# Optimization experiments

Hardware: AMD Instinct MI355X
Metric: run time of the kernel (lower is better)

## Reference

```python
import jax, jax.numpy as jnp
import numpy as np

C = 512
CQK = C // 8
B, H, W = 4, 128, 128

def setup_inputs() -> dict:
    key = jax.random.key(0)
    ks = jax.random.split(key, 8)
    x = jax.random.normal(ks[0], (B, C, H, W), dtype=jnp.float32)
    # 1x1 conv weights stored as [out, in]
    Wq = jax.random.normal(ks[1], (CQK, C), dtype=jnp.float32) * (1.0 / np.sqrt(C))
    bq = jax.random.normal(ks[2], (CQK,), dtype=jnp.float32) * 0.01
    Wk = jax.random.normal(ks[3], (CQK, C), dtype=jnp.float32) * (1.0 / np.sqrt(C))
    bk = jax.random.normal(ks[4], (CQK,), dtype=jnp.float32) * 0.01
    Wv = jax.random.normal(ks[5], (C, C), dtype=jnp.float32) * (1.0 / np.sqrt(C))
    bv = jax.random.normal(ks[6], (C,), dtype=jnp.float32) * 0.01
    gamma = jnp.zeros((1,), dtype=jnp.float32)
    return {"x": x, "Wq": Wq, "bq": bq, "Wk": Wk, "bk": bk, "Wv": Wv, "bv": bv, "gamma": gamma}

def _conv1x1(x, Wt, b):
    # x: [B,C,H,W], Wt: [O,C] -> [B,O,H,W]
    return jnp.einsum('bchw,oc->bohw', x, Wt) + b[None, :, None, None]

def reference(x, Wq, bq, Wk, bk, Wv, bv, gamma):
    q = _conv1x1(x, Wq, bq)   # [B,CQK,H,W]
    k = _conv1x1(x, Wk, bk)   # [B,CQK,H,W]
    v = _conv1x1(x, Wv, bv)   # [B,C,H,W]
    # axial attention along height, independently per (batch, width-column)
    energy = jnp.einsum('bchw,bcgw->bwhg', q, k)      # [B,W,H,H]
    attn = jax.nn.softmax(energy, axis=-1)
    out = jnp.einsum('bcgw,bwhg->bchw', v, attn)      # [B,C,H,W]
    return gamma * out + x
```

## Files before the change

kernel.cpp:

```cpp
#include <hip/hip_runtime.h>
#include <hip/hip_bf16.h>

typedef float f32x4  __attribute__((ext_vector_type(4)));
typedef short s16x8  __attribute__((ext_vector_type(8)));
typedef unsigned short u16;
typedef unsigned char  u8;

#define B_ 4
#define C_ 512
#define H_ 128
#define W_ 128
#define NO_ 640

__device__ __forceinline__ u16 f2bf(float f) {
    __hip_bfloat16 h = __float2bfloat16(f);
    union { __hip_bfloat16 h; u16 u; } cv; cv.h = h; return cv.u;
}
__device__ __forceinline__ unsigned f2fp8x2(float a, float b) {
    return (unsigned)__builtin_amdgcn_cvt_pk_fp8_f32(a, b, 0, false);
}
__device__ __forceinline__ u8 f2fp8(float f) {
    return (u8)(f2fp8x2(f, 0.f) & 0xFF);
}
__device__ __forceinline__ float fp82f(unsigned b) {
    const unsigned s = (b >> 7) & 1u, e = (b >> 3) & 15u, m = b & 7u;
    union { unsigned u; float f; } c;
    c.u = (s << 31) | ((e + 120u) << 23) | (m << 20);
    const float fs = (s ? -1.f : 1.f) * (float)m * 0.001953125f;
    return e ? c.f : fs;
}

__device__ __forceinline__ void gld16(const void* g, void* l) {
    __builtin_amdgcn_global_load_lds(
        (const __attribute__((address_space(1))) void*)g,
        (__attribute__((address_space(3))) void*)l, 16, 0, 0);
}

__global__ __launch_bounds__(256) void k_convw(const float* __restrict__ Wq, const float* __restrict__ bq,
                                               const float* __restrict__ Wk, const float* __restrict__ bk,
                                               const float* __restrict__ Wv, const float* __restrict__ bv,
                                               u8* __restrict__ Wcat, float* __restrict__ bcat) {
    const int idx = blockIdx.x * 256 + threadIdx.x;
    if (idx < NO_ * C_) {
        const int o = idx >> 9, c = idx & 511;
        float v;
        if (o < 64)       v = Wq[o * C_ + c];
        else if (o < 128) v = Wk[(o - 64) * C_ + c];
        else              v = Wv[(o - 128) * C_ + c];
        Wcat[idx] = f2fp8(v);
    }
    if (idx < NO_) {
        float v = (idx < 64) ? bq[idx] : ((idx < 128) ? bk[idx - 64] : bv[idx - 128]);
        bcat[idx] = v;
    }
}

__global__ __launch_bounds__(256) void k_transpose_x(const float* __restrict__ x, u8* __restrict__ xT) {
    __shared__ float tile[64][65];
    const int b  = blockIdx.x >> 7;
    const int h  = blockIdx.x & 127;
    const int c0 = (blockIdx.y >> 1) * 64;
    const int w0 = (blockIdx.y & 1) * 64;
    const int t = threadIdx.x, r = t >> 4, seg = t & 15;
    const float* xp = x + (size_t)b * C_ * H_ * W_ + (size_t)h * W_;
#pragma unroll
    for (int rr = 0; rr < 4; ++rr) {
        const int c = rr * 16 + r;
        float4 v = *(const float4*)(xp + (size_t)(c0 + c) * (H_ * W_) + w0 + seg * 4);
        tile[c][seg * 4 + 0] = v.x; tile[c][seg * 4 + 1] = v.y;
        tile[c][seg * 4 + 2] = v.z; tile[c][seg * 4 + 3] = v.w;
    }
    __syncthreads();
#pragma unroll
    for (int rr = 0; rr < 4; ++rr) {
        const int w = rr * 16 + r;
        const unsigned lo = f2fp8x2(tile[seg * 4 + 0][w], tile[seg * 4 + 1][w]);
        const unsigned hi = f2fp8x2(tile[seg * 4 + 2][w], tile[seg * 4 + 3][w]);
        *(unsigned*)(xT + ((size_t)((b * W_ + w0 + w) * H_ + h)) * C_ + c0 + seg * 4)
            = (lo & 0xFFFFu) | (hi << 16);
    }
}

__global__ __launch_bounds__(256, 4) void k_gemm(const u8* __restrict__ A, const u8* __restrict__ Wc,
                                                 const float* __restrict__ bias, u8* __restrict__ Call,
                                                 u8* __restrict__ vt) {
    __shared__ __align__(16) u8 smem[32768];
    const int t = threadIdx.x;
    const int lane = t & 63;
    const int wave = t >> 6;
    const int wr = wave >> 1;
    const int wc = wave & 1;
    const int lr = lane & 15;
    const int q4 = lane >> 4;

    const int bid = blockIdx.x;
    const int wg = (bid & 7) * 320 + (bid >> 3);
    const int panel = wg / 5;
    const int n = wg - panel * 5;
    const int r0 = panel * 128;
    const int n0 = n * 128;

    const int srow = t >> 2;
    const int slog = (t & 3) ^ ((srow >> 1) & 3);
    const u8* gA = A  + (size_t)(r0 + srow) * C_ + slog * 16;
    const u8* gB = Wc + (size_t)(n0 + srow) * C_ + slog * 16;

#define STAGE(KT) do {                                               \
        u8* S_ = smem + ((KT) & 1) * 16384;                          \
        const int k0_ = (KT) * 64;                                   \
        gld16(gA + k0_,                   S_ + t * 16);              \
        gld16(gA + (size_t)64 * C_ + k0_, S_ + 4096  + t * 16);      \
        gld16(gB + k0_,                   S_ + 8192  + t * 16);      \
        gld16(gB + (size_t)64 * C_ + k0_, S_ + 12288 + t * 16);      \
    } while (0)

    f32x4 acc[4][4] = {};
    STAGE(0);

#pragma unroll
    for (int T = 0; T < 8; ++T) {
        asm volatile("s_waitcnt vmcnt(0)" ::: "memory");
        __builtin_amdgcn_s_barrier();
        const u8* Ab = smem + (T & 1) * 16384;
        const u8* Bb = Ab + 8192;
        long fa[2][4], fb[2][4];
#pragma unroll
        for (int ks = 0; ks < 2; ++ks) {
            const int lbase = ks * 2 + (q4 >> 1);
            const int boff  = (q4 & 1) * 8;
#pragma unroll
            for (int mi = 0; mi < 4; ++mi) {
                const int rr = wr * 64 + mi * 16 + lr;
                fa[ks][mi] = *(const long*)&Ab[rr * 64 + ((lbase ^ ((rr >> 1) & 3)) * 16) + boff];
            }
#pragma unroll
            for (int ni = 0; ni < 4; ++ni) {
                const int rr = wc * 64 + ni * 16 + lr;
                fb[ks][ni] = *(const long*)&Bb[rr * 64 + ((lbase ^ ((rr >> 1) & 3)) * 16) + boff];
            }
        }
        if (T < 7) STAGE(T + 1);
        __builtin_amdgcn_s_setprio(1);
#pragma unroll
        for (int ks = 0; ks < 2; ++ks)
#pragma unroll
            for (int mi = 0; mi < 4; ++mi)
#pragma unroll
                for (int ni = 0; ni < 4; ++ni)
                    acc[mi][ni] = __builtin_amdgcn_mfma_f32_16x16x32_fp8_fp8(
                        fa[ks][mi], fb[ks][ni], acc[mi][ni], 0, 0, 0);
        __builtin_amdgcn_s_setprio(0);
    }
#undef STAGE
    __syncthreads();

    if (n == 0) {
#pragma unroll
        for (int ni = 0; ni < 4; ++ni) {
            const int o = wc * 64 + ni * 16 + lr;
            const float bz = bias[o];
#pragma unroll
            for (int mi = 0; mi < 4; ++mi)
#pragma unroll
                for (int j = 0; j < 4; ++j) {
                    const int rg = r0 + wr * 64 + mi * 16 + q4 * 4 + j;
                    Call[(size_t)rg * 128 + o] = f2fp8(acc[mi][ni][j] + bz);
                }
        }
    } else {
        u8* Tt = smem;
#pragma unroll
        for (int ni = 0; ni < 4; ++ni) {
            const int c_loc = wc * 64 + ni * 16 + lr;
            const float bz = bias[n0 + c_loc];
#pragma unroll
            for (int mi = 0; mi < 4; ++mi) {
                const int h = wr * 64 + mi * 16 + q4 * 4;
                unsigned p = f2fp8x2(acc[mi][ni][0] + bz, acc[mi][ni][1] + bz) & 0xFFFFu;
                p |= f2fp8x2(acc[mi][ni][2] + bz, acc[mi][ni][3] + bz) << 16;
                *(unsigned*)&Tt[c_loc * 144 + h] = p;
            }
        }
        __syncthreads();
        {
            const int c_loc = t >> 1;
            const int half  = t & 1;
            const int cg = (n - 1) * 128 + c_loc;
            u8* dst = vt + ((size_t)panel * 512 + cg) * 128 + half * 64;
            const u8* src = &Tt[c_loc * 144 + half * 64];
#pragma unroll
            for (int k = 0; k < 4; ++k)
                *(int4*)&dst[k * 16] = *(const int4*)&src[k * 16];
        }
    }
}

__global__ __launch_bounds__(256) void k_attn(const u8* __restrict__ Call, const u8* __restrict__ vt,
                                              u8* __restrict__ outws) {
    __shared__ __align__(16) float E[128][132];
    __shared__ float Rinv[128];
    const int bw = blockIdx.x;
    const int t = threadIdx.x;
    const int lane = t & 63;
    const int wr = t >> 7;
    const int wc = (t >> 6) & 1;
    const int lr = lane & 15, lk = (lane >> 4) * 8;
    const size_t rowbase = (size_t)bw * 128;

    f32x4 e[4][4] = {};
#pragma unroll
    for (int kk = 0; kk < 2; ++kk) {
        long fq[4], fk[4];
#pragma unroll
        for (int mi = 0; mi < 4; ++mi)
            fq[mi] = *(const long*)&Call[(rowbase + wr * 64 + mi * 16 + lr) * 128 + kk * 32 + lk];
#pragma unroll
        for (int ni = 0; ni < 4; ++ni)
            fk[ni] = *(const long*)&Call[(rowbase + wc * 64 + ni * 16 + lr) * 128 + 64 + kk * 32 + lk];
#pragma unroll
        for (int mi = 0; mi < 4; ++mi)
#pragma unroll
            for (int ni = 0; ni < 4; ++ni)
                e[mi][ni] = __builtin_amdgcn_mfma_f32_16x16x32_fp8_fp8(fq[mi], fk[ni], e[mi][ni], 0, 0, 0);
    }
#pragma unroll
    for (int mi = 0; mi < 4; ++mi)
#pragma unroll
        for (int ni = 0; ni < 4; ++ni)
#pragma unroll
            for (int j = 0; j < 4; ++j)
                E[wr * 64 + mi * 16 + (lane >> 4) * 4 + j][wc * 64 + ni * 16 + lr] = e[mi][ni][j];
    __syncthreads();

    {
        const int h = t >> 1, hf = (t & 1) * 64;
        float m = -1e30f;
        for (int i = 0; i < 64; ++i) m = fmaxf(m, E[h][hf + i]);
        m = fmaxf(m, __shfl_xor(m, 1));
        float s = 0.f;
        for (int i = 0; i < 64; ++i) {
            float p = __expf(E[h][hf + i] - m);
            E[h][hf + i] = p;
            s += p;
        }
        s += __shfl_xor(s, 1);
        if ((t & 1) == 0) Rinv[h] = 1.0f / s;
    }
    __syncthreads();

    float rv[4][4];
#pragma unroll
    for (int mi = 0; mi < 4; ++mi)
#pragma unroll
        for (int j = 0; j < 4; ++j)
            rv[mi][j] = Rinv[wr * 64 + mi * 16 + (lane >> 4) * 4 + j];

    long pa[4][4];
#pragma unroll
    for (int kk = 0; kk < 4; ++kk)
#pragma unroll
        for (int mi = 0; mi < 4; ++mi) {
            const float* ep = &E[wr * 64 + mi * 16 + lr][kk * 32 + lk];
            float4 v0 = *(const float4*)ep;
            float4 v1 = *(const float4*)(ep + 4);
            unsigned lo = (unsigned)__builtin_amdgcn_cvt_pk_fp8_f32(v0.x, v0.y, 0, false);
            lo = (unsigned)__builtin_amdgcn_cvt_pk_fp8_f32(v0.z, v0.w, (int)lo, true);
            unsigned hi = (unsigned)__builtin_amdgcn_cvt_pk_fp8_f32(v1.x, v1.y, 0, false);
            hi = (unsigned)__builtin_amdgcn_cvt_pk_fp8_f32(v1.z, v1.w, (int)hi, true);
            pa[kk][mi] = (long)lo | ((long)hi << 32);
        }

    for (int cc = 0; cc < 4; ++cc) {
        f32x4 acc[4][4] = {};
#pragma unroll
        for (int kk = 0; kk < 4; ++kk) {
            long fb[4];
#pragma unroll
            for (int ni = 0; ni < 4; ++ni)
                fb[ni] = *(const long*)&vt[((size_t)bw * 512 + cc * 128 + wc * 64 + ni * 16 + lr) * 128 + kk * 32 + lk];
#pragma unroll
            for (int mi = 0; mi < 4; ++mi)
#pragma unroll
                for (int ni = 0; ni < 4; ++ni)
                    acc[mi][ni] = __builtin_amdgcn_mfma_f32_16x16x32_fp8_fp8(pa[kk][mi], fb[ni], acc[mi][ni], 0, 0, 0);
        }
#pragma unroll
        for (int ni = 0; ni < 4; ++ni) {
            const int c = cc * 128 + wc * 64 + ni * 16 + lr;
#pragma unroll
            for (int mi = 0; mi < 4; ++mi)
#pragma unroll
                for (int j = 0; j < 4; ++j) {
                    const int hh = wr * 64 + mi * 16 + (lane >> 4) * 4 + j;
                    outws[(rowbase + hh) * 512 + c] = f2fp8(acc[mi][ni][j] * rv[mi][j]);
                }
        }
    }
}

__global__ __launch_bounds__(256) void k_merge(const u8* __restrict__ outws, const float* __restrict__ x,
                                               const float* __restrict__ gamma, float* __restrict__ out) {
    __shared__ float tile[64][65];
    const int b  = blockIdx.x >> 7;
    const int h  = blockIdx.x & 127;
    const int c0 = (blockIdx.y >> 1) * 64;
    const int w0 = (blockIdx.y & 1) * 64;
    const float g = gamma[0];
    const int t = threadIdx.x, r = t >> 4, seg = t & 15;
#pragma unroll
    for (int rr = 0; rr < 4; ++rr) {
        const int w = rr * 16 + r;
        unsigned v = *(const unsigned*)(outws + ((size_t)((b * W_ + w0 + w) * H_) + h) * C_ + c0 + seg * 4);
        tile[w][seg * 4 + 0] = fp82f(v & 0xFFu);
        tile[w][seg * 4 + 1] = fp82f((v >> 8) & 0xFFu);
        tile[w][seg * 4 + 2] = fp82f((v >> 16) & 0xFFu);
        tile[w][seg * 4 + 3] = fp82f(v >> 24);
    }
    __syncthreads();
#pragma unroll
    for (int rr = 0; rr < 4; ++rr) {
        const int c = rr * 16 + r;
        const size_t base = ((size_t)(b * C_ + c0 + c) * H_ + h) * W_ + w0 + seg * 4;
        float4 xv = *(const float4*)(x + base);
        float4 o;
        o.x = g * tile[seg * 4 + 0][c] + xv.x;
        o.y = g * tile[seg * 4 + 1][c] + xv.y;
        o.z = g * tile[seg * 4 + 2][c] + xv.z;
        o.w = g * tile[seg * 4 + 3][c] + xv.w;
        *(float4*)(out + base) = o;
    }
}

extern "C" void kernel_launch(void* const* d_in, const int* in_sizes, int n_in,
                              void* d_out, int out_size, void* d_ws, size_t ws_size,
                              hipStream_t stream) {
    const float* x     = (const float*)d_in[0];
    const float* Wq    = (const float*)d_in[1];
    const float* bq    = (const float*)d_in[2];
    const float* Wk    = (const float*)d_in[3];
    const float* bk    = (const float*)d_in[4];
    const float* Wv    = (const float*)d_in[5];
    const float* bv    = (const float*)d_in[6];
    const float* gamma = (const float*)d_in[7];

    char* ws = (char*)d_ws;
    u8*    Wcat  = (u8*)ws;
    float* bcat  = (float*)(ws + 655360);
    u8*    xT    = (u8*)(ws + (1u << 20));
    u8*    Call  = (u8*)(ws + (1u << 20) + 67108864);
    u8*    outws = (u8*)(ws + (1u << 20));
    u8*    vt    = (u8*)d_out;

    k_convw<<<dim3((NO_ * C_ + 255) / 256), 256, 0, stream>>>(Wq, bq, Wk, bk, Wv, bv, Wcat, bcat);
    k_transpose_x<<<dim3(B_ * H_, 16), 256, 0, stream>>>(x, xT);
    k_gemm<<<dim3(2560), 256, 0, stream>>>(xT, Wcat, bcat, Call, vt);
    k_attn<<<dim3(B_ * W_), 256, 0, stream>>>(Call, vt, outws);
    k_merge<<<dim3(B_ * H_, 16), 256, 0, stream>>>(outws, x, gamma, (float*)d_out);
}
```

Baseline: 155.8 us.

## Use 16x16x128 scaled FP8 MFMA with 128-wide K tiles in projection GEMM

Replaces the 16x16x32 FP8 MFMA with the gfx950 scaled 16x16x128 f8f6f4 MFMA, using unit scales (0x7F exponent). The K tile grows from 64 to 128, so the main loop runs four iterations instead of eight, with a new 8-way XOR swizzle and 16-byte LDS reads. Shared memory doubles to 64KB and launch bounds drop to 2 blocks per SM. The aim is fewer MFMA issues and fewer barriers, at the cost of lower occupancy.

```diff
diff --git a/kernel.cpp b/kernel.cpp
--- a/kernel.cpp
+++ b/kernel.cpp
@@ -2,7 +2,7 @@
 #include <hip/hip_bf16.h>
 
 typedef float f32x4  __attribute__((ext_vector_type(4)));
-typedef short s16x8  __attribute__((ext_vector_type(8)));
+typedef int   v8i    __attribute__((ext_vector_type(8)));
 typedef unsigned short u16;
 typedef unsigned char  u8;
 
@@ -81,10 +81,10 @@
     }
 }
 
-__global__ __launch_bounds__(256, 4) void k_gemm(const u8* __restrict__ A, const u8* __restrict__ Wc,
+__global__ __launch_bounds__(256, 2) void k_gemm(const u8* __restrict__ A, const u8* __restrict__ Wc,
                                                  const float* __restrict__ bias, u8* __restrict__ Call,
                                                  u8* __restrict__ vt) {
-    __shared__ __align__(16) u8 smem[32768];
+    __shared__ __align__(16) u8 smem[65536];
     const int t = threadIdx.x;
     const int lane = t & 63;
     const int wave = t >> 6;
@@ -100,55 +100,63 @@
     const int r0 = panel * 128;
     const int n0 = n * 128;
 
-    const int srow = t >> 2;
-    const int slog = (t & 3) ^ ((srow >> 1) & 3);
+    const int srow = t >> 3;
+    const int slog = (t & 7) ^ (srow & 7);
     const u8* gA = A  + (size_t)(r0 + srow) * C_ + slog * 16;
     const u8* gB = Wc + (size_t)(n0 + srow) * C_ + slog * 16;
 
-#define STAGE(KT) do {                                               \
-        u8* S_ = smem + ((KT) & 1) * 16384;                          \
-        const int k0_ = (KT) * 64;                                   \
-        gld16(gA + k0_,                   S_ + t * 16);              \
-        gld16(gA + (size_t)64 * C_ + k0_, S_ + 4096  + t * 16);      \
-        gld16(gB + k0_,                   S_ + 8192  + t * 16);      \
-        gld16(gB + (size_t)64 * C_ + k0_, S_ + 12288 + t * 16);      \
+#define STAGE(KT) do {                                                   \
+        u8* S_ = smem + ((KT) & 1) * 32768;                              \
+        const int k0_ = (KT) * 128;                                      \
+        gld16(gA + k0_,                    S_ + t * 16);                 \
+        gld16(gA + (size_t)32 * C_ + k0_,  S_ + 4096  + t * 16);         \
+        gld16(gA + (size_t)64 * C_ + k0_,  S_ + 8192  + t * 16);         \
+        gld16(gA + (size_t)96 * C_ + k0_,  S_ + 12288 + t * 16);         \
+        gld16(gB + k0_,                    S_ + 16384 + t * 16);         \
+        gld16(gB + (size_t)32 * C_ + k0_,  S_ + 20480 + t * 16);         \
+        gld16(gB + (size_t)64 * C_ + k0_,  S_ + 24576 + t * 16);         \
+        gld16(gB + (size_t)96 * C_ + k0_,  S_ + 28672 + t * 16);         \
     } while (0)
 
     f32x4 acc[4][4] = {};
     STAGE(0);
 
 #pragma unroll
-    for (int T = 0; T < 8; ++T) {
+    for (int T = 0; T < 4; ++T) {
         asm volatile("s_waitcnt vmcnt(0)" ::: "memory");
         __builtin_amdgcn_s_barrier();
-        const u8* Ab = smem + (T & 1) * 16384;
-        const u8* Bb = Ab + 8192;
-        long fa[2][4], fb[2][4];
-#pragma unroll
-        for (int ks = 0; ks < 2; ++ks) {
-            const int lbase = ks * 2 + (q4 >> 1);
-            const int boff  = (q4 & 1) * 8;
-#pragma unroll
-            for (int mi = 0; mi < 4; ++mi) {
-                const int rr = wr * 64 + mi * 16 + lr;
-                fa[ks][mi] = *(const long*)&Ab[rr * 64 + ((lbase ^ ((rr >> 1) & 3)) * 16) + boff];
-            }
-#pragma unroll
-            for (int ni = 0; ni < 4; ++ni) {
-                const int rr = wc * 64 + ni * 16 + lr;
-                fb[ks][ni] = *(const long*)&Bb[rr * 64 + ((lbase ^ ((rr >> 1) & 3)) * 16) + boff];
-            }
-        }
-        if (T < 7) STAGE(T + 1);
+        const u8* Ab = smem + (T & 1) * 32768;
+        const u8* Bb = Ab + 16384;
+        v8i fa[4], fb[4];
+#pragma unroll
+        for (int mi = 0; mi < 4; ++mi) {
+            const int rr = wr * 64 + mi * 16 + lr;
+            int4 lo = *(const int4*)&Ab[rr * 128 + (((2 * q4 + 0) ^ (rr & 7)) * 16)];
+            int4 hi = *(const int4*)&Ab[rr * 128 + (((2 * q4 + 1) ^ (rr & 7)) * 16)];
+            v8i f; f[0] = lo.x; f[1] = lo.y; f[2] = lo.z; f[3] = lo.w;
+                   f[4] = hi.x; f[5] = hi.y; f[6] = hi.z; f[7] = hi.w;
+            fa[mi] = f;
+        }
+#pragma unroll
+        for (int ni = 0; ni < 4; ++ni) {
+            const int rr = wc * 64 + ni * 16 + lr;
+            int4 lo = *(const int4*)&Bb[rr * 128 + (((2 * q4 + 0) ^ (rr & 7)) * 16)];
+            int4 hi = *(const int4*)&Bb[rr * 128 + (((2 * q4 + 1) ^ (rr & 7)) * 16)];
+            v8i f; f[0] = lo.x; f[1] = lo.y; f[2] = lo.z; f[3] = lo.w;
+                   f[4] = hi.x; f[5] = hi.y; f[6] = hi.z; f[7] = hi.w;
+            fb[ni] = f;
+        }
+        if (T < 3) STAGE(T + 1);
         __builtin_amdgcn_s_setprio(1);
 #pragma unroll
-        for (int ks = 0; ks < 2; ++ks)
-#pragma unroll
-            for (int mi = 0; mi < 4; ++mi)
-#pragma unroll
-                for (int ni = 0; ni < 4; ++ni)
-                    acc[mi][ni] = __builtin_amdgcn_mfma_f32_16x16x32_fp8_fp8(
-                        fa[ks][mi], fb[ks][ni], acc[mi][ni], 0, 0, 0);
+        for (int mi = 0; mi < 4; ++mi)
+#pragma unroll
+            for (int ni = 0; ni < 4; ++ni)
+                acc[mi][ni] = __builtin_amdgcn_mfma_scale_f32_16x16x128_f8f6f4(
+                    fa[mi], fb[ni], acc[mi][ni],
+                    0, 0,
+                    0, 0x7F7F7F7Fu,
+                    0, 0x7F7F7F7Fu);
         __builtin_amdgcn_s_setprio(0);
     }
 #undef STAGE
```

Measured after the change: 154.5 us, median of 3. About the same (-0.9%).
